# Performance work log

Measured on AMD Instinct MI355X. Metric: run time of the kernel, lower is better.

## Reference

```python
import jax, jax.numpy as jnp
import numpy as np

B, T, F, H, L = 256, 512, 64, 256, 2
DH = 2 * H          # decoder hidden size (bidirectional encoder concat)
OUT, OSL = 2, 20    # output_size, output_seq_len


def gru_cell(x, h, Wih, Whh, bih, bhh):
    # PyTorch GRU cell, gate order (r, z, n)
    gi = x @ Wih.T + bih
    gh = h @ Whh.T + bhh
    ir, iz, inn = jnp.split(gi, 3, axis=-1)
    hr, hz, hn = jnp.split(gh, 3, axis=-1)
    r = jax.nn.sigmoid(ir + hr)
    z = jax.nn.sigmoid(iz + hz)
    n = jnp.tanh(inn + r * hn)
    return (1.0 - z) * n + z * h


def setup_inputs() -> dict:
    key = jax.random.key(0)
    ks = iter(jax.random.split(key, 32))
    def p(shape, scale=0.05):
        return jax.random.normal(next(ks), shape, dtype=jnp.float32) * scale
    inp = {
        "x": p((B, T, F), 1.0),
        "start_token": jnp.zeros((1, 1, OUT), jnp.float32),
        # encoder layer 0 (input F), layer 1 (input 2H); axis 0 = direction (fwd, bwd)
        "enc_Wih0": p((2, 3 * H, F)), "enc_Whh0": p((2, 3 * H, H)),
        "enc_bih0": p((2, 3 * H)),   "enc_bhh0": p((2, 3 * H)),
        "enc_Wih1": p((2, 3 * H, 2 * H)), "enc_Whh1": p((2, 3 * H, H)),
        "enc_bih1": p((2, 3 * H)),   "enc_bhh1": p((2, 3 * H)),
        # decoder: unidirectional, hidden DH; layer0 input OUT, layer1 input DH
        "dec_Wih0": p((3 * DH, OUT)), "dec_Whh0": p((3 * DH, DH)),
        "dec_bih0": p((3 * DH,)),    "dec_bhh0": p((3 * DH,)),
        "dec_Wih1": p((3 * DH, DH)), "dec_Whh1": p((3 * DH, DH)),
        "dec_bih1": p((3 * DH,)),    "dec_bhh1": p((3 * DH,)),
        "fc_W": p((OUT, DH)), "fc_b": p((OUT,)),
    }
    return inp


def _run_dir(xs, Wih, Whh, bih, bhh, reverse):
    # xs: [T, B, Fin] -> (ys [T, B, H], h_T [B, H])
    h0 = jnp.zeros((xs.shape[1], Whh.shape[1]), xs.dtype)
    def step(h, xt):
        hn = gru_cell(xt, h, Wih, Whh, bih, bhh)
        return hn, hn
    hT, ys = jax.lax.scan(step, h0, xs, reverse=reverse)
    return ys, hT


def reference(x, start_token,
              enc_Wih0, enc_Whh0, enc_bih0, enc_bhh0,
              enc_Wih1, enc_Whh1, enc_bih1, enc_bhh1,
              dec_Wih0, dec_Whh0, dec_bih0, dec_bhh0,
              dec_Wih1, dec_Whh1, dec_bih1, dec_bhh1,
              fc_W, fc_b):
    b = x.shape[0]
    xs = jnp.swapaxes(x, 0, 1)  # [T, B, F]
    enc_layers = [(enc_Wih0, enc_Whh0, enc_bih0, enc_bhh0),
                  (enc_Wih1, enc_Whh1, enc_bih1, enc_bhh1)]
    hiddens = []
    layer_in = xs
    for (Wih, Whh, bih, bhh) in enc_layers:
        yf, hf = _run_dir(layer_in, Wih[0], Whh[0], bih[0], bhh[0], reverse=False)
        yb, hb = _run_dir(layer_in, Wih[1], Whh[1], bih[1], bhh[1], reverse=True)
        layer_in = jnp.concatenate([yf, yb], axis=-1)   # [T, B, 2H]
        hiddens.append(jnp.concatenate([hf, hb], axis=-1))  # [B, 2H] = cat(fwd, bwd)
    inp0 = jnp.broadcast_to(start_token, (b, 1, OUT))[:, 0]  # [B, OUT]
    def dec_step(carry, _):
        inp, (h0, h1) = carry
        h0n = gru_cell(inp, h0, dec_Wih0, dec_Whh0, dec_bih0, dec_bhh0)
        h1n = gru_cell(h0n, h1, dec_Wih1, dec_Whh1, dec_bih1, dec_bhh1)
        pred = h1n @ fc_W.T + fc_b
        return (pred, (h0n, h1n)), pred
    _, preds = jax.lax.scan(dec_step, (inp0, (hiddens[0], hiddens[1])), None, length=OSL)
    return jnp.swapaxes(preds, 0, 1)  # [B, OSL, OUT]
```

## Files before the change

### kernel.cpp

```cpp
#include <hip/hip_runtime.h>
#include <hip/hip_bf16.h>
#include <stdint.h>
#include <stddef.h>


typedef __bf16 bf16_t;
typedef bf16_t bf16x8 __attribute__((ext_vector_type(8)));
typedef float  f32x4  __attribute__((ext_vector_type(4)));

#define B_   256
#define T_   512
#define F_   64
#define H_   256
#define G_   768
#define DH_  512
#define DG_  1536
#define OSL_ 20

__device__ __forceinline__ float sigm(float x) {
    float e = __builtin_amdgcn_exp2f(-1.442695040888963f * x);
    return __builtin_amdgcn_rcpf(1.0f + e);
}
__device__ __forceinline__ float tanh_(float x) {
    float e = __builtin_amdgcn_exp2f(-2.885390081777927f * x);
    return __builtin_amdgcn_rcpf(1.0f + e) * 2.0f - 1.0f;
}

__device__ __forceinline__ bf16x8 load_f32x8_as_bf16(const float* p) {
    f32x4 u = *(const f32x4*)p;
    f32x4 v = *(const f32x4*)(p + 4);
    bf16x8 r;
    r[0]=(bf16_t)u[0]; r[1]=(bf16_t)u[1]; r[2]=(bf16_t)u[2]; r[3]=(bf16_t)u[3];
    r[4]=(bf16_t)v[0]; r[5]=(bf16_t)v[1]; r[6]=(bf16_t)v[2]; r[7]=(bf16_t)v[3];
    return r;
}


__global__ void cast_f32_bf16(const float* __restrict__ src, bf16_t* __restrict__ dst, int n) {
    int i = blockIdx.x * 256 + threadIdx.x;
    if (i < n) dst[i] = (bf16_t)src[i];
}

__global__ void weff_prep(const float* __restrict__ wih0d, const float* __restrict__ fcw,
                          const float* __restrict__ fcb, const float* __restrict__ bih0d,
                          const float* __restrict__ st, bf16_t* __restrict__ weff,
                          float* __restrict__ beff, float* __restrict__ ov) {
    int tid = blockIdx.x * 256 + threadIdx.x;
    if (tid >= DG_ * DH_) return;
    int g = tid >> 9, k = tid & 511;
    float a0 = wih0d[g * 2], a1 = wih0d[g * 2 + 1];
    weff[tid] = (bf16_t)(a0 * fcw[k] + a1 * fcw[DH_ + k]);
    if (k == 0) {
        beff[g] = a0 * fcb[0] + a1 * fcb[1] + bih0d[g];
        ov[g]   = a0 * st[0]  + a1 * st[1]  + bih0d[g];
    }
}

__global__ __launch_bounds__(256) void gemm_gi(
    const float* __restrict__ x, const bf16_t* __restrict__ xcat,
    const bf16_t* __restrict__ Bt, bf16_t* __restrict__ gi, int t0, int K) {
    __shared__ bf16_t As[128 * 64];
    __shared__ bf16_t Bs[128 * 64];
    int m0 = blockIdx.x * 128, n0 = blockIdx.y * 128;
    int tid = threadIdx.x;
    int lane = tid & 63, w = tid >> 6;
    int col = lane & 15, quad = lane >> 4;
    int qm = (w >> 1) * 64, qn = (w & 1) * 64;

    int tl = m0 >> 8;
    int bbase = m0 & 255;
    int t_real = t0 + tl;
    if (n0 >= 768) t_real = (T_ - 1) - t_real;

    f32x4 acc[4][4] = {};
    for (int k0 = 0; k0 < K; k0 += 64) {
        __syncthreads();
#pragma unroll
        for (int i = 0; i < 4; i++) {
            int c = i * 256 + tid;
            int m = c >> 3, kc = c & 7;
            int kcs = kc ^ (m & 7);
            bf16x8 av;
            if (K == 64) {
                av = load_f32x8_as_bf16(x + ((size_t)(bbase + m) * T_ + t_real) * F_ + kcs * 8);
            } else {
                av = *(const bf16x8*)(xcat + ((size_t)t_real * B_ + bbase + m) * DH_ + k0 + kcs * 8);
            }
            *(bf16x8*)(&As[c * 8]) = av;
            *(bf16x8*)(&Bs[c * 8]) = *(const bf16x8*)(Bt + (size_t)(n0 + m) * K + k0 + kcs * 8);
        }
        __syncthreads();
#pragma unroll
        for (int kt = 0; kt < 2; kt++) {
            bf16x8 a[4], b[4];
#pragma unroll
            for (int mt = 0; mt < 4; mt++) {
                int r = qm + mt * 16 + col;
                a[mt] = *(const bf16x8*)(&As[(r * 8 + ((kt * 4 + quad) ^ (r & 7))) * 8]);
                int rn = qn + mt * 16 + col;
                b[mt] = *(const bf16x8*)(&Bs[(rn * 8 + ((kt * 4 + quad) ^ (rn & 7))) * 8]);
            }
#pragma unroll
            for (int mt = 0; mt < 4; mt++)
#pragma unroll
                for (int nt = 0; nt < 4; nt++)
                    acc[mt][nt] = __builtin_amdgcn_mfma_f32_16x16x32_bf16(a[mt], b[nt], acc[mt][nt], 0, 0, 0);
        }
    }
#pragma unroll
    for (int mt = 0; mt < 4; mt++)
#pragma unroll
        for (int nt = 0; nt < 4; nt++)
#pragma unroll
            for (int i = 0; i < 4; i++) {
                int row = m0 + qm + mt * 16 + quad * 4 + i;
                int cg  = n0 + qn + nt * 16 + col;
                gi[(size_t)row * DG_ + cg] = (bf16_t)acc[mt][nt][i];
            }
}

__global__ __launch_bounds__(512) void gru_scan(
    const bf16_t* __restrict__ gi, int t0, int tc,
    const bf16_t* __restrict__ whh,
    const float* __restrict__ bih, const float* __restrict__ bhh,
    float* __restrict__ hstate, bf16_t* __restrict__ y, float* __restrict__ hT) {
    __shared__ bf16_t gi_lds[16 * 768];
    __shared__ bf16_t h_lds[2 * 16 * 264];

    int dir = blockIdx.x >> 4;
    int b0  = (blockIdx.x & 15) * 16;
    int tid = threadIdx.x;
    int w = tid >> 6, lane = tid & 63, col = lane & 15, quad = lane >> 4;

    bf16x8 wf[3][2][8];
    const bf16_t* wbase = whh + (size_t)dir * G_ * H_;
#pragma unroll
    for (int g = 0; g < 3; g++)
#pragma unroll
        for (int nt = 0; nt < 2; nt++) {
            int row = g * 256 + w * 32 + nt * 16 + col;
#pragma unroll
            for (int kt = 0; kt < 8; kt++)
                wf[g][nt][kt] = *(const bf16x8*)(wbase + (size_t)row * H_ + kt * 32 + quad * 8);
        }
    float brz[2][2], bin_[2], bhn[2];
#pragma unroll
    for (int nt = 0; nt < 2; nt++) {
        int j = w * 32 + nt * 16 + col;
        brz[0][nt] = bih[dir * G_ + j] + bhh[dir * G_ + j];
        brz[1][nt] = bih[dir * G_ + 256 + j] + bhh[dir * G_ + 256 + j];
        bin_[nt]   = bih[dir * G_ + 512 + j];
        bhn[nt]    = bhh[dir * G_ + 512 + j];
    }
    int bb[3], oo[3];
#pragma unroll
    for (int it = 0; it < 3; it++) {
        int c = it * 512 + tid;
        bb[it] = c / 96;
        oo[it] = (c % 96) * 8;
    }
    float hold[2][4];
#pragma unroll
    for (int nt = 0; nt < 2; nt++)
#pragma unroll
        for (int i = 0; i < 4; i++) {
            int j = w * 32 + nt * 16 + col;
            hold[nt][i] = t0 ? hstate[dir * 65536 + (b0 + quad * 4 + i) * 256 + j] : 0.0f;
        }
    for (int i = tid; i < 16 * 264; i += 512) {
        int b = i / 264, j = i % 264;
        float v = (t0 && j < 256) ? hstate[dir * 65536 + (b0 + b) * 256 + j] : 0.0f;
        h_lds[i] = (bf16_t)v;
    }
#pragma unroll
    for (int it = 0; it < 3; it++) {
        int c = it * 512 + tid;
        *(bf16x8*)(&gi_lds[c * 8]) =
            *(const bf16x8*)(gi + ((size_t)0 * B_ + b0 + bb[it]) * DG_ + dir * G_ + oo[it]);
    }
    __syncthreads();

    for (int s = 0; s < tc; s++) {
        int par = s & 1;
        int t = t0 + s;
        int sn = (s + 1 < tc) ? (s + 1) : s;

        bf16x8 pg[3];
#pragma unroll
        for (int it = 0; it < 3; it++)
            pg[it] = *(const bf16x8*)(gi + ((size_t)sn * B_ + b0 + bb[it]) * DG_ + dir * G_ + oo[it]);

        f32x4 acc[3][2] = {};
        const bf16_t* hcur = &h_lds[par * 4224];
#pragma unroll
        for (int kt = 0; kt < 8; kt++) {
            bf16x8 af = *(const bf16x8*)(hcur + col * 264 + kt * 32 + quad * 8);
#pragma unroll
            for (int g = 0; g < 3; g++)
#pragma unroll
                for (int nt = 0; nt < 2; nt++)
                    acc[g][nt] = __builtin_amdgcn_mfma_f32_16x16x32_bf16(af, wf[g][nt][kt], acc[g][nt], 0, 0, 0);
        }

        bf16_t* hnext = &h_lds[(par ^ 1) * 4224];
        int tp = dir ? (T_ - 1 - t) : t;
#pragma unroll
        for (int nt = 0; nt < 2; nt++) {
            int j = w * 32 + nt * 16 + col;
#pragma unroll
            for (int i = 0; i < 4; i++) {
                int b = quad * 4 + i;
                float gr = acc[0][nt][i] + (float)gi_lds[b * 768 + j]       + brz[0][nt];
                float gz = acc[1][nt][i] + (float)gi_lds[b * 768 + 256 + j] + brz[1][nt];
                float gn = (float)gi_lds[b * 768 + 512 + j] + bin_[nt];
                float r = sigm(gr), z = sigm(gz);
                float n = tanh_(gn + r * (acc[2][nt][i] + bhn[nt]));
                float hv = (1.0f - z) * n + z * hold[nt][i];
                hold[nt][i] = hv;
                hnext[b * 264 + j] = (bf16_t)hv;
                if (y) y[((size_t)tp * B_ + b0 + b) * DH_ + dir * H_ + j] = (bf16_t)hv;
                if (t == T_ - 1) hT[(size_t)(b0 + b) * DH_ + dir * H_ + j] = hv;
            }
        }
        __syncthreads();
#pragma unroll
        for (int it = 0; it < 3; it++)
            *(bf16x8*)(&gi_lds[(it * 512 + tid) * 8]) = pg[it];
        __syncthreads();
    }
#pragma unroll
    for (int nt = 0; nt < 2; nt++)
#pragma unroll
        for (int i = 0; i < 4; i++) {
            int j = w * 32 + nt * 16 + col;
            hstate[dir * 65536 + (b0 + quad * 4 + i) * 256 + j] = hold[nt][i];
        }
}

__global__ __launch_bounds__(256) void dec_cell(
    const float* __restrict__ xsrc, const bf16_t* __restrict__ Wx,
    const float* __restrict__ bx, const float* __restrict__ ov,
    const float* __restrict__ hin, const bf16_t* __restrict__ Wh,
    const float* __restrict__ bh, float* __restrict__ hout,
    float* __restrict__ hist) {
    int jblk = blockIdx.x & 7;
    int b0   = (blockIdx.x >> 3) * 16;
    int tid = threadIdx.x, w = tid >> 6, lane = tid & 63, col = lane & 15, quad = lane >> 4;
    int j = jblk * 64 + w * 16 + col;
    bool do_gi = (ov == nullptr);

    f32x4 agi[3] = {}, agh[3] = {};
#pragma unroll 4
    for (int kt = 0; kt < 16; kt++) {
        bf16x8 ah = load_f32x8_as_bf16(hin + (size_t)(b0 + col) * DH_ + kt * 32 + quad * 8);
#pragma unroll
        for (int g = 0; g < 3; g++) {
            bf16x8 bw = *(const bf16x8*)(Wh + (size_t)(g * DH_ + j) * DH_ + kt * 32 + quad * 8);
            agh[g] = __builtin_amdgcn_mfma_f32_16x16x32_bf16(ah, bw, agh[g], 0, 0, 0);
        }
        if (do_gi) {
            bf16x8 ax = load_f32x8_as_bf16(xsrc + (size_t)(b0 + col) * DH_ + kt * 32 + quad * 8);
#pragma unroll
            for (int g = 0; g < 3; g++) {
                bf16x8 bw = *(const bf16x8*)(Wx + (size_t)(g * DH_ + j) * DH_ + kt * 32 + quad * 8);
                agi[g] = __builtin_amdgcn_mfma_f32_16x16x32_bf16(ax, bw, agi[g], 0, 0, 0);
            }
        }
    }
#pragma unroll
    for (int i = 0; i < 4; i++) {
        int b = b0 + quad * 4 + i;
        float gr, gz, gn;
        if (do_gi) {
            gr = agi[0][i] + bx[j];
            gz = agi[1][i] + bx[DH_ + j];
            gn = agi[2][i] + bx[2 * DH_ + j];
        } else {
            gr = ov[j]; gz = ov[DH_ + j]; gn = ov[2 * DH_ + j];
        }
        float hr = agh[0][i] + bh[j];
        float hz = agh[1][i] + bh[DH_ + j];
        float hn = agh[2][i] + bh[2 * DH_ + j];
        float r = sigm(gr + hr), z = sigm(gz + hz);
        float n = tanh_(gn + r * hn);
        float hold = hin[(size_t)b * DH_ + j];
        float hv = (1.0f - z) * n + z * hold;
        hout[(size_t)b * DH_ + j] = hv;
        if (hist) hist[(size_t)b * DH_ + j] = hv;
    }
}

__global__ __launch_bounds__(256) void fc_all(
    const float* __restrict__ hist, const float* __restrict__ fcw,
    const float* __restrict__ fcb, float* __restrict__ out) {
    int t  = blockIdx.x >> 4;
    int b0 = (blockIdx.x & 15) * 16;
    int tid = threadIdx.x;
    int bl = tid >> 4, o = (tid >> 3) & 1, part = tid & 7;
    const float* hp = hist + ((size_t)t * B_ + b0 + bl) * DH_;
    const float* wp = fcw + o * DH_;
    float s = 0.0f;
    for (int k = part * 64; k < part * 64 + 64; k += 4) {
        f32x4 hv = *(const f32x4*)(hp + k);
        f32x4 wv = *(const f32x4*)(wp + k);
        s += hv[0] * wv[0] + hv[1] * wv[1] + hv[2] * wv[2] + hv[3] * wv[3];
    }
    s += __shfl_down(s, 4); s += __shfl_down(s, 2); s += __shfl_down(s, 1);
    if (part == 0) out[(size_t)(b0 + bl) * (OSL_ * 2) + t * 2 + o] = s + fcb[o];
}


#define OFF_WIH0E 0ull
#define OFF_WHH0E 196608ull
#define OFF_WIH1E 983040ull
#define OFF_WHH1E 2555904ull
#define OFF_WDHH0 3342336ull
#define OFF_WDIH1 4915200ull
#define OFF_WDHH1 6488064ull
#define OFF_WEFF  8060928ull
#define OFF_BEFF  9633792ull
#define OFF_OV    9658368ull
#define OFF_H0A   9682944ull
#define OFF_H0B   10207232ull
#define OFF_H1A   10731520ull
#define OFF_H1B   11255808ull
#define OFF_HST   11780096ull
#define OFF_HIST  12304384ull
#define OFF_XCAT  22790144ull
#define OFF_GI    157007872ull

extern "C" void kernel_launch(void* const* d_in, const int* in_sizes, int n_in,
                              void* d_out, int out_size, void* d_ws, size_t ws_size,
                              hipStream_t stream) {
    const float* x      = (const float*)d_in[0];
    const float* st     = (const float*)d_in[1];
    const float* eWih0  = (const float*)d_in[2];
    const float* eWhh0  = (const float*)d_in[3];
    const float* ebih0  = (const float*)d_in[4];
    const float* ebhh0  = (const float*)d_in[5];
    const float* eWih1  = (const float*)d_in[6];
    const float* eWhh1  = (const float*)d_in[7];
    const float* ebih1  = (const float*)d_in[8];
    const float* ebhh1  = (const float*)d_in[9];
    const float* dWih0  = (const float*)d_in[10];
    const float* dWhh0  = (const float*)d_in[11];
    const float* dbih0  = (const float*)d_in[12];
    const float* dbhh0  = (const float*)d_in[13];
    const float* dWih1  = (const float*)d_in[14];
    const float* dWhh1  = (const float*)d_in[15];
    const float* dbih1  = (const float*)d_in[16];
    const float* dbhh1  = (const float*)d_in[17];
    const float* fcW    = (const float*)d_in[18];
    const float* fcb    = (const float*)d_in[19];

    char* ws = (char*)d_ws;
    bf16_t* wih0e = (bf16_t*)(ws + OFF_WIH0E);
    bf16_t* whh0e = (bf16_t*)(ws + OFF_WHH0E);
    bf16_t* wih1e = (bf16_t*)(ws + OFF_WIH1E);
    bf16_t* whh1e = (bf16_t*)(ws + OFF_WHH1E);
    bf16_t* wdhh0 = (bf16_t*)(ws + OFF_WDHH0);
    bf16_t* wdih1 = (bf16_t*)(ws + OFF_WDIH1);
    bf16_t* wdhh1 = (bf16_t*)(ws + OFF_WDHH1);
    bf16_t* weff  = (bf16_t*)(ws + OFF_WEFF);
    float*  beff  = (float*)(ws + OFF_BEFF);
    float*  ovp   = (float*)(ws + OFF_OV);
    float*  h0buf[2] = { (float*)(ws + OFF_H0A), (float*)(ws + OFF_H0B) };
    float*  h1buf[2] = { (float*)(ws + OFF_H1A), (float*)(ws + OFF_H1B) };
    float*  hstate = (float*)(ws + OFF_HST);
    float*  hist  = (float*)(ws + OFF_HIST);
    bf16_t* xcat  = (bf16_t*)(ws + OFF_XCAT);
    bf16_t* gi    = (bf16_t*)(ws + OFF_GI);

    int Tc = 512;
    while (Tc > 8 && OFF_GI + (unsigned long long)Tc * 786432ull > (unsigned long long)ws_size)
        Tc >>= 1;
    int nch = T_ / Tc;

    cast_f32_bf16<<<(2*G_*F_ + 255)/256, 256, 0, stream>>>(eWih0, wih0e, 2*G_*F_);
    cast_f32_bf16<<<(2*G_*H_ + 255)/256, 256, 0, stream>>>(eWhh0, whh0e, 2*G_*H_);
    cast_f32_bf16<<<(2*G_*DH_ + 255)/256, 256, 0, stream>>>(eWih1, wih1e, 2*G_*DH_);
    cast_f32_bf16<<<(2*G_*H_ + 255)/256, 256, 0, stream>>>(eWhh1, whh1e, 2*G_*H_);
    cast_f32_bf16<<<(DG_*DH_ + 255)/256, 256, 0, stream>>>(dWhh0, wdhh0, DG_*DH_);
    cast_f32_bf16<<<(DG_*DH_ + 255)/256, 256, 0, stream>>>(dWih1, wdih1, DG_*DH_);
    cast_f32_bf16<<<(DG_*DH_ + 255)/256, 256, 0, stream>>>(dWhh1, wdhh1, DG_*DH_);
    weff_prep<<<(DG_*DH_ + 255)/256, 256, 0, stream>>>(dWih0, fcW, fcb, dbih0, st, weff, beff, ovp);

    for (int c = 0; c < nch; c++) {
        gemm_gi<<<dim3(Tc * 2, 12), 256, 0, stream>>>(x, nullptr, wih0e, gi, c * Tc, 64);
        gru_scan<<<32, 512, 0, stream>>>(gi, c * Tc, Tc, whh0e, ebih0, ebhh0, hstate, xcat, h0buf[0]);
    }
    for (int c = 0; c < nch; c++) {
        gemm_gi<<<dim3(Tc * 2, 12), 256, 0, stream>>>(nullptr, xcat, wih1e, gi, c * Tc, 512);
        gru_scan<<<32, 512, 0, stream>>>(gi, c * Tc, Tc, whh1e, ebih1, ebhh1, hstate, nullptr, h1buf[0]);
    }

    int p0 = 0, p1 = 0;
    for (int t = 0; t < OSL_; t++) {
        dec_cell<<<128, 256, 0, stream>>>(h1buf[p1], weff, beff, (t == 0 ? ovp : nullptr),
                                          h0buf[p0], wdhh0, dbhh0, h0buf[p0 ^ 1], nullptr);
        p0 ^= 1;
        dec_cell<<<128, 256, 0, stream>>>(h0buf[p0], wdih1, dbih1, nullptr,
                                          h1buf[p1], wdhh1, dbhh1, h1buf[p1 ^ 1],
                                          hist + (size_t)t * B_ * DH_);
        p1 ^= 1;
    }
    fc_all<<<OSL_ * 16, 256, 0, stream>>>(hist, fcW, fcb, (float*)d_out);
}
```

Before: 4.892 ms.

## Fuse decoder steps into persistent kernel with per-batch-group atomic barriers

The 40 per-step decoder launches are replaced by one persistent kernel of 128 blocks. Each group of 8 blocks that shares a 16-row batch slice syncs through a global atomic counter barrier with a spin timeout. The eight weight-cast and prep kernels are merged into one 2D-grid launch, which also zeroes the barrier counters. This removes launch gaps and fixed per-launch cost. It relies on all 128 blocks being resident at once, and the spin timeout could in principle let a block proceed before its group has finished.

```diff
diff --git a/kernel.cpp b/kernel.cpp
--- a/kernel.cpp
+++ b/kernel.cpp
@@ -35,24 +35,40 @@
     return r;
 }
 
-
-__global__ void cast_f32_bf16(const float* __restrict__ src, bf16_t* __restrict__ dst, int n) {
+__global__ __launch_bounds__(256) void prep_all(
+    const float* __restrict__ s0, const float* __restrict__ s1,
+    const float* __restrict__ s2, const float* __restrict__ s3,
+    const float* __restrict__ s4, const float* __restrict__ s5,
+    const float* __restrict__ s6,
+    bf16_t* __restrict__ d0, bf16_t* __restrict__ d1, bf16_t* __restrict__ d2,
+    bf16_t* __restrict__ d3, bf16_t* __restrict__ d4, bf16_t* __restrict__ d5,
+    bf16_t* __restrict__ d6,
+    const float* __restrict__ wih0d, const float* __restrict__ fcw,
+    const float* __restrict__ fcb, const float* __restrict__ bih0d,
+    const float* __restrict__ st, bf16_t* __restrict__ weff,
+    float* __restrict__ beff, float* __restrict__ ov,
+    unsigned int* __restrict__ bar) {
     int i = blockIdx.x * 256 + threadIdx.x;
-    if (i < n) dst[i] = (bf16_t)src[i];
-}
-
-__global__ void weff_prep(const float* __restrict__ wih0d, const float* __restrict__ fcw,
-                          const float* __restrict__ fcb, const float* __restrict__ bih0d,
-                          const float* __restrict__ st, bf16_t* __restrict__ weff,
-                          float* __restrict__ beff, float* __restrict__ ov) {
-    int tid = blockIdx.x * 256 + threadIdx.x;
-    if (tid >= DG_ * DH_) return;
-    int g = tid >> 9, k = tid & 511;
-    float a0 = wih0d[g * 2], a1 = wih0d[g * 2 + 1];
-    weff[tid] = (bf16_t)(a0 * fcw[k] + a1 * fcw[DH_ + k]);
-    if (k == 0) {
-        beff[g] = a0 * fcb[0] + a1 * fcb[1] + bih0d[g];
-        ov[g]   = a0 * st[0]  + a1 * st[1]  + bih0d[g];
+    switch (blockIdx.y) {
+      case 0: if (i < 2*G_*F_)  d0[i] = (bf16_t)s0[i]; break;
+      case 1: if (i < 2*G_*H_)  d1[i] = (bf16_t)s1[i]; break;
+      case 2: if (i < 2*G_*DH_) d2[i] = (bf16_t)s2[i]; break;
+      case 3: if (i < 2*G_*H_)  d3[i] = (bf16_t)s3[i]; break;
+      case 4: if (i < DG_*DH_)  d4[i] = (bf16_t)s4[i]; break;
+      case 5: if (i < DG_*DH_)  d5[i] = (bf16_t)s5[i]; break;
+      case 6: if (i < DG_*DH_)  d6[i] = (bf16_t)s6[i]; break;
+      default: {
+        if (i < 40 * 16) bar[i] = 0u;
+        if (i < DG_*DH_) {
+          int g = i >> 9, k = i & 511;
+          float a0 = wih0d[g * 2], a1 = wih0d[g * 2 + 1];
+          weff[i] = (bf16_t)(a0 * fcw[k] + a1 * fcw[DH_ + k]);
+          if (k == 0) {
+            beff[g] = a0 * fcb[0] + a1 * fcb[1] + bih0d[g];
+            ov[g]   = a0 * st[0]  + a1 * st[1]  + bih0d[g];
+          }
+        }
+      } break;
     }
 }
 
@@ -237,18 +253,30 @@
         }
 }
 
-__global__ __launch_bounds__(256) void dec_cell(
+
+__device__ __forceinline__ void group_barrier(unsigned int* cnt) {
+    __threadfence();
+    __syncthreads();
+    if (threadIdx.x == 0) {
+        unsigned int old = atomicAdd(cnt, 1u);
+        if (old < 7u) {
+            unsigned int spins = 0;
+            while (atomicAdd(cnt, 0u) < 8u && ++spins < (1u << 18))
+                __builtin_amdgcn_s_sleep(1);
+        }
+    }
+    __syncthreads();
+    __threadfence();
+}
+
+__device__ __forceinline__ void dec_cell_body(
+    int b0, int j, int quad, int col,
     const float* __restrict__ xsrc, const bf16_t* __restrict__ Wx,
-    const float* __restrict__ bx, const float* __restrict__ ov,
+    const float* __restrict__ bx, const float* __restrict__ ovv,
     const float* __restrict__ hin, const bf16_t* __restrict__ Wh,
     const float* __restrict__ bh, float* __restrict__ hout,
     float* __restrict__ hist) {
-    int jblk = blockIdx.x & 7;
-    int b0   = (blockIdx.x >> 3) * 16;
-    int tid = threadIdx.x, w = tid >> 6, lane = tid & 63, col = lane & 15, quad = lane >> 4;
-    int j = jblk * 64 + w * 16 + col;
-    bool do_gi = (ov == nullptr);
-
+    bool do_gi = (ovv == nullptr);
     f32x4 agi[3] = {}, agh[3] = {};
 #pragma unroll 4
     for (int kt = 0; kt < 16; kt++) {
@@ -276,7 +304,7 @@
             gz = agi[1][i] + bx[DH_ + j];
             gn = agi[2][i] + bx[2 * DH_ + j];
         } else {
-            gr = ov[j]; gz = ov[DH_ + j]; gn = ov[2 * DH_ + j];
+            gr = ovv[j]; gz = ovv[DH_ + j]; gn = ovv[2 * DH_ + j];
         }
         float hr = agh[0][i] + bh[j];
         float hz = agh[1][i] + bh[DH_ + j];
@@ -287,6 +315,38 @@
         float hv = (1.0f - z) * n + z * hold;
         hout[(size_t)b * DH_ + j] = hv;
         if (hist) hist[(size_t)b * DH_ + j] = hv;
+    }
+}
+
+__global__ __launch_bounds__(256) void dec_fused(
+    const bf16_t* __restrict__ weff, const float* __restrict__ beff,
+    const float* __restrict__ ov,
+    const bf16_t* __restrict__ wdhh0, const float* __restrict__ dbhh0,
+    const bf16_t* __restrict__ wdih1, const float* __restrict__ dbih1,
+    const bf16_t* __restrict__ wdhh1, const float* __restrict__ dbhh1,
+    float* h0a, float* h0b, float* h1a, float* h1b,
+    float* __restrict__ hist, unsigned int* __restrict__ bar) {
+    int grp  = blockIdx.x & 15;
+    int b0 = grp * 16;
+    int tid = threadIdx.x, w = tid >> 6, lane = tid & 63;
+    int col = lane & 15, quad = lane >> 4;
+    int j = (blockIdx.x >> 4) * 64 + w * 16 + col;
+
+    float *h0c = h0a, *h0n = h0b, *h1c = h1a, *h1n = h1b;
+    int ph = 0;
+    for (int t = 0; t < OSL_; t++) {
+        dec_cell_body(b0, j, quad, col,
+                      h1c, weff, beff, (t == 0 ? ov : nullptr),
+                      h0c, wdhh0, dbhh0, h0n, nullptr);
+        { float* tmp = h0c; h0c = h0n; h0n = tmp; }
+        group_barrier(bar + (ph++) * 16 + grp);
+
+        dec_cell_body(b0, j, quad, col,
+                      h0c, wdih1, dbih1, nullptr,
+                      h1c, wdhh1, dbhh1, h1n,
+                      hist + (size_t)t * B_ * DH_);
+        { float* tmp = h1c; h1c = h1n; h1n = tmp; }
+        if (t < OSL_ - 1) group_barrier(bar + (ph++) * 16 + grp);
     }
 }
 
@@ -319,6 +379,7 @@
 #define OFF_WDHH1 6488064ull
 #define OFF_WEFF  8060928ull
 #define OFF_BEFF  9633792ull
+#define OFF_BAR   9641984ull
 #define OFF_OV    9658368ull
 #define OFF_H0A   9682944ull
 #define OFF_H0B   10207232ull
@@ -363,6 +424,7 @@
     bf16_t* wdhh1 = (bf16_t*)(ws + OFF_WDHH1);
     bf16_t* weff  = (bf16_t*)(ws + OFF_WEFF);
     float*  beff  = (float*)(ws + OFF_BEFF);
+    unsigned int* bar = (unsigned int*)(ws + OFF_BAR);
     float*  ovp   = (float*)(ws + OFF_OV);
     float*  h0buf[2] = { (float*)(ws + OFF_H0A), (float*)(ws + OFF_H0B) };
     float*  h1buf[2] = { (float*)(ws + OFF_H1A), (float*)(ws + OFF_H1B) };
@@ -376,14 +438,10 @@
         Tc >>= 1;
     int nch = T_ / Tc;
 
-    cast_f32_bf16<<<(2*G_*F_ + 255)/256, 256, 0, stream>>>(eWih0, wih0e, 2*G_*F_);
-    cast_f32_bf16<<<(2*G_*H_ + 255)/256, 256, 0, stream>>>(eWhh0, whh0e, 2*G_*H_);
-    cast_f32_bf16<<<(2*G_*DH_ + 255)/256, 256, 0, stream>>>(eWih1, wih1e, 2*G_*DH_);
-    cast_f32_bf16<<<(2*G_*H_ + 255)/256, 256, 0, stream>>>(eWhh1, whh1e, 2*G_*H_);
-    cast_f32_bf16<<<(DG_*DH_ + 255)/256, 256, 0, stream>>>(dWhh0, wdhh0, DG_*DH_);
-    cast_f32_bf16<<<(DG_*DH_ + 255)/256, 256, 0, stream>>>(dWih1, wdih1, DG_*DH_);
-    cast_f32_bf16<<<(DG_*DH_ + 255)/256, 256, 0, stream>>>(dWhh1, wdhh1, DG_*DH_);
-    weff_prep<<<(DG_*DH_ + 255)/256, 256, 0, stream>>>(dWih0, fcW, fcb, dbih0, st, weff, beff, ovp);
+    prep_all<<<dim3(3072, 8), 256, 0, stream>>>(
+        eWih0, eWhh0, eWih1, eWhh1, dWhh0, dWih1, dWhh1,
+        wih0e, whh0e, wih1e, whh1e, wdhh0, wdih1, wdhh1,
+        dWih0, fcW, fcb, dbih0, st, weff, beff, ovp, bar);
 
     for (int c = 0; c < nch; c++) {
         gemm_gi<<<dim3(Tc * 2, 12), 256, 0, stream>>>(x, nullptr, wih0e, gi, c * Tc, 64);
@@ -394,15 +452,10 @@
         gru_scan<<<32, 512, 0, stream>>>(gi, c * Tc, Tc, whh1e, ebih1, ebhh1, hstate, nullptr, h1buf[0]);
     }
 
-    int p0 = 0, p1 = 0;
-    for (int t = 0; t < OSL_; t++) {
-        dec_cell<<<128, 256, 0, stream>>>(h1buf[p1], weff, beff, (t == 0 ? ovp : nullptr),
-                                          h0buf[p0], wdhh0, dbhh0, h0buf[p0 ^ 1], nullptr);
-        p0 ^= 1;
-        dec_cell<<<128, 256, 0, stream>>>(h0buf[p0], wdih1, dbih1, nullptr,
-                                          h1buf[p1], wdhh1, dbhh1, h1buf[p1 ^ 1],
-                                          hist + (size_t)t * B_ * DH_);
-        p1 ^= 1;
-    }
+    dec_fused<<<128, 256, 0, stream>>>(weff, beff, ovp,
+                                       wdhh0, dbhh0, wdih1, dbih1, wdhh1, dbhh1,
+                                       h0buf[0], h0buf[1], h1buf[0], h1buf[1],
+                                       hist, bar);
+
     fc_all<<<OSL_ * 16, 256, 0, stream>>>(hist, fcW, fcb, (float*)d_out);
 }
```

Measured after the change: 5.704 ms. 16.6% more time.
